# Kernel optimization log

Measured on AMD Instinct MI355X. Metric: run time of the kernel, lower is better.

The kernel has to match this reference:

```python
import jax, jax.numpy as jnp
import numpy as np

N_ENT = 100000
N_REL = 100
DIM = 128
N_BASES = 10
N_LAYERS = 2
N_EDGES = 600000


def setup_inputs() -> dict:
    key = jax.random.key(0)
    ks = jax.random.split(key, 8)
    source = jax.random.randint(ks[0], (N_EDGES,), 0, N_ENT)
    target = jax.random.randint(ks[1], (N_EDGES,), 0, N_ENT)
    edge_type = jax.random.randint(ks[2], (N_EDGES,), 0, N_REL)
    x0 = jax.random.normal(ks[3], (N_ENT, DIM), dtype=jnp.float32)
    bases = jax.random.normal(ks[4], (N_BASES, DIM, DIM), dtype=jnp.float32) * (DIM ** -0.5)
    coefs = jax.random.normal(ks[5], (N_LAYERS, N_REL, N_BASES), dtype=jnp.float32) * (N_BASES ** -0.5)
    self_w = jax.random.normal(ks[6], (N_LAYERS, DIM, DIM), dtype=jnp.float32) * (DIM ** -0.5)
    bias = jnp.zeros((N_LAYERS, DIM), dtype=jnp.float32)
    return {"x0": x0, "bases": bases, "coefs": coefs, "self_w": self_w,
            "bias": bias, "source": source, "target": target, "edge_type": edge_type}


def reference(x0, bases, coefs, self_w, bias, source, target, edge_type):
    """R-GCN entity representations (basis decomposition, inverse in-degree norm).

    x0: (N, d) base entity embeddings; bases: (B, d, d); coefs: (L, R, B);
    self_w: (L, d, d); bias: (L, d); source/target/edge_type: (E,) int.
    Returns (N, d) entity representations after L layers.
    """
    n = x0.shape[0]
    n_layers = coefs.shape[0]
    n_bases = bases.shape[0]
    # inverse in-degree edge weights: w_e = 1 / indegree(target_e)
    indeg = jax.ops.segment_sum(jnp.ones_like(target, dtype=x0.dtype), target, num_segments=n)
    ew = (1.0 / jnp.maximum(indeg, 1.0))[target]  # (E,)
    x = x0
    for l in range(n_layers):
        xs = x[source]                         # (E, d) gather
        ecoef = coefs[l][edge_type]            # (E, B) relation-specific basis coefficients
        msg = jnp.zeros_like(xs)
        for b in range(n_bases):               # small fixed loop over bases
            msg = msg + ecoef[:, b:b + 1] * (xs @ bases[b])
        agg = jax.ops.segment_sum(ew[:, None] * msg, target, num_segments=n)  # (N, d)
        x = jax.nn.relu(agg + x @ self_w[l] + bias[l])
    return x
```

## Files before the change

kernel.cpp:

```cpp
#include <hip/hip_runtime.h>

#define NENT    100000
#define NENTPAD 100096
#define NREL    100
#define DIM     128
#define NBASES  10
#define NEDGES  600000
#define CH      128
#define TMAX    4788
#define PADE    612736
#define NB_ESCAN 98
#define EPB     4096
#define NBH     147

typedef unsigned short u16;
typedef unsigned int   u32;
typedef __bf16  bf16x8 __attribute__((ext_vector_type(8)));
typedef float   f32x16 __attribute__((ext_vector_type(16)));

static __device__ __forceinline__ u16 f2bf(float f) {
  u32 u = __float_as_uint(f);
  u = (u + 0x7fffu + ((u >> 16) & 1u)) >> 16;
  return (u16)u;
}
static __device__ __forceinline__ float bf2f(u32 h) {
  return __uint_as_float(h << 16);
}
static __device__ __forceinline__ u32 pk2(float a, float b) {
  return (u32)f2bf(a) | ((u32)f2bf(b) << 16);
}
#define GLD16(g, l) __builtin_amdgcn_global_load_lds( \
    (__attribute__((address_space(1))) u32*)(g), \
    (__attribute__((address_space(3))) u32*)(l), 16, 0, 0)

__global__ __launch_bounds__(1024) void k_hist2(const int* __restrict__ tgt,
                                                const int* __restrict__ rel,
                                                int* __restrict__ indeg,
                                                int* __restrict__ hist) {
  __shared__ int h[NREL];
  int tid = threadIdx.x, blk = blockIdx.x;
  if (tid < NREL) h[tid] = 0;
  __syncthreads();
  int base = blk * EPB;
  int nv = NEDGES - base; if (nv > EPB) nv = EPB;
#pragma unroll
  for (int k = 0; k < 4; ++k) {
    int j = tid + k * 1024;
    if (j < nv) {
      int i = base + j;
      atomicAdd(&indeg[tgt[i]], 1);
      atomicAdd(&h[rel[i]], 1);
    }
  }
  __syncthreads();
  if (tid < NREL) hist[tid * NBH + blk] = h[tid];
}

__global__ __launch_bounds__(1024) void k_scan2(int* __restrict__ hist,
                                                int* __restrict__ chunk_rel,
                                                int* __restrict__ chunk_start,
                                                int* __restrict__ chunk_valid,
                                                int* __restrict__ chunkT) {
  __shared__ int sh[NREL * NBH];
  __shared__ int cnt[NREL];
  __shared__ int cb[128];
  int tid = threadIdx.x;
  for (int i = tid; i < NREL * NBH; i += 1024) sh[i] = hist[i];
  __syncthreads();
  if (tid < NREL) {
    int s = 0;
    for (int b = 0; b < NBH; ++b) s += sh[tid * NBH + b];
    cnt[tid] = s;
  }
  __syncthreads();
  if (tid < 128) cb[tid] = (tid < NREL) ? (cnt[tid] + CH - 1) / CH : 0;
  __syncthreads();
  for (int d = 1; d < 128; d <<= 1) {
    int t = 0;
    if (tid < 128 && tid >= d) t = cb[tid - d];
    __syncthreads();
    if (tid < 128) cb[tid] += t;
    __syncthreads();
  }
  if (tid < NREL) {
    int c = cnt[tid];
    int nch = (c + CH - 1) / CH;
    int cb0 = cb[tid] - nch;
    int poff = cb0 * CH;
    for (int i = 0; i < nch; ++i) {
      chunk_rel[cb0 + i] = tid;
      chunk_start[cb0 + i] = (cb0 + i) * CH;
      int v = c - i * CH;
      if (v > CH) v = CH;
      chunk_valid[cb0 + i] = v;
    }
    int run = poff;
    for (int b = 0; b < NBH; ++b) {
      int t = sh[tid * NBH + b];
      sh[tid * NBH + b] = run;
      run += t;
    }
  }
  if (tid == 127) *chunkT = cb[127];
  __syncthreads();
  for (int i = tid; i < NREL * NBH; i += 1024) hist[i] = sh[i];
}

__global__ __launch_bounds__(1024) void k_scatter2(const int* __restrict__ src,
                                                   const int* __restrict__ tgt,
                                                   const int* __restrict__ rel,
                                                   const int* __restrict__ hist,
                                                   const int* __restrict__ row_ptr,
                                                   int* __restrict__ fill_t,
                                                   int* __restrict__ es,
                                                   int* __restrict__ tp) {
  __shared__ int lh[NREL];
  __shared__ int lc[NREL];
  __shared__ int goff[NREL];
  __shared__ int ls[128];
  __shared__ int es_l[EPB];
  __shared__ int tp_l[EPB];
  __shared__ int dst_l[EPB];
  int tid = threadIdx.x, blk = blockIdx.x;
  int base = blk * EPB;
  int nv = NEDGES - base; if (nv > EPB) nv = EPB;
  if (tid < NREL) {
    lh[tid] = 0; lc[tid] = 0;
    goff[tid] = hist[tid * NBH + blk];
  }
  __syncthreads();
  int r4[4], s4[4], t4[4];
#pragma unroll
  for (int k = 0; k < 4; ++k) {
    int j = tid + k * 1024;
    if (j < nv) {
      int i = base + j;
      r4[k] = rel[i]; s4[k] = src[i]; t4[k] = tgt[i];
      atomicAdd(&lh[r4[k]], 1);
    } else r4[k] = -1;
  }
  __syncthreads();
  if (tid < 128) ls[tid] = (tid < NREL) ? lh[tid] : 0;
  __syncthreads();
  for (int d = 1; d < 128; d <<= 1) {
    int t = 0;
    if (tid < 128 && tid >= d) t = ls[tid - d];
    __syncthreads();
    if (tid < 128) ls[tid] += t;
    __syncthreads();
  }
#pragma unroll
  for (int k = 0; k < 4; ++k) {
    if (r4[k] >= 0) {
      int r = r4[k];
      int rank = atomicAdd(&lc[r], 1);
      int lpos = ls[r] - lh[r] + rank;
      es_l[lpos] = s4[k];
      dst_l[lpos] = goff[r] + rank;
      tp_l[lpos] = row_ptr[t4[k]] + atomicAdd(&fill_t[t4[k]], 1);
    }
  }
  __syncthreads();
  for (int j = tid; j < nv; j += 1024) {
    int d = dst_l[j];
    es[d] = es_l[j];
    tp[d] = tp_l[j];
  }
}

__global__ void k_escanA(const int* __restrict__ indeg, int* __restrict__ loc,
                         int* __restrict__ bsum) {
  __shared__ int s[256];
  int tid = threadIdx.x;
  int base = blockIdx.x * 1024 + tid * 4;
  int v0 = (base + 0 < NENT) ? indeg[base + 0] : 0;
  int v1 = (base + 1 < NENT) ? indeg[base + 1] : 0;
  int v2 = (base + 2 < NENT) ? indeg[base + 2] : 0;
  int v3 = (base + 3 < NENT) ? indeg[base + 3] : 0;
  s[tid] = v0 + v1 + v2 + v3;
  __syncthreads();
  for (int d = 1; d < 256; d <<= 1) {
    int t = (tid >= d) ? s[tid - d] : 0;
    __syncthreads();
    s[tid] += t;
    __syncthreads();
  }
  int off = (tid > 0) ? s[tid - 1] : 0;
  if (base + 0 < NENT) loc[base + 0] = off;
  if (base + 1 < NENT) loc[base + 1] = off + v0;
  if (base + 2 < NENT) loc[base + 2] = off + v0 + v1;
  if (base + 3 < NENT) loc[base + 3] = off + v0 + v1 + v2;
  if (tid == 255) bsum[blockIdx.x] = s[255];
}

__global__ void k_escanB(int* __restrict__ bsum) {
  __shared__ int s[128];
  int tid = threadIdx.x;
  s[tid] = (tid < NB_ESCAN) ? bsum[tid] : 0;
  __syncthreads();
  for (int d = 1; d < 128; d <<= 1) {
    int t = (tid >= d) ? s[tid - d] : 0;
    __syncthreads();
    s[tid] += t;
    __syncthreads();
  }
  if (tid < NB_ESCAN) bsum[tid] = (tid > 0) ? s[tid - 1] : 0;
}

__global__ void k_escanC(const int* __restrict__ loc, const int* __restrict__ bsum,
                         int* __restrict__ row_ptr) {
  int i = blockIdx.x * blockDim.x + threadIdx.x;
  if (i < NENT) row_ptr[i] = loc[i] + bsum[i >> 10];
}

__global__ void k_tobf(const float* __restrict__ x, u16* __restrict__ xbf) {
  int t = blockIdx.x * 256 + threadIdx.x;
  int row = t >> 4, g = t & 15;
  int c = g ^ (row & 7);
  const float4* xr = (const float4*)(x + (size_t)row * DIM + c * 8);
  float4 a = xr[0], b = xr[1];
  uint4 o;
  o.x = pk2(a.x, a.y); o.y = pk2(a.z, a.w);
  o.z = pk2(b.x, b.y); o.w = pk2(b.z, b.w);
  *(uint4*)(xbf + (size_t)row * DIM + g * 8) = o;
}

__global__ void k_wmatT(const float* __restrict__ bases, const float* __restrict__ coefs_l,
                        u16* __restrict__ Wt) {
  int g = blockIdx.x * 256 + threadIdx.x;
  int r = g >> 11;
  int rem = g & 2047;
  int k8 = rem >> 7;
  int dim = rem & 127;
  float cf[NBASES];
#pragma unroll
  for (int bb = 0; bb < NBASES; ++bb) cf[bb] = coefs_l[r * NBASES + bb];
  float v[8];
#pragma unroll
  for (int i = 0; i < 8; ++i) v[i] = 0.f;
  for (int bb = 0; bb < NBASES; ++bb) {
    const float* bp = bases + (size_t)bb * DIM * DIM + (k8 * 8) * DIM + dim;
#pragma unroll
    for (int i = 0; i < 8; ++i) v[i] += cf[bb] * bp[i * DIM];
  }
  uint4 o;
  o.x = pk2(v[0], v[1]); o.y = pk2(v[2], v[3]);
  o.z = pk2(v[4], v[5]); o.w = pk2(v[6], v[7]);
  *(uint4*)(Wt + (size_t)r * DIM * DIM + dim * DIM + ((k8 ^ (dim & 7)) * 8)) = o;
}

__global__ void k_swtT(const float* __restrict__ sw, u16* __restrict__ swt) {
  int g = blockIdx.x * 256 + threadIdx.x;
  int ll = g >> 11;
  int rem = g & 2047;
  int k8 = rem >> 7;
  int dim = rem & 127;
  const float* bp = sw + (size_t)ll * DIM * DIM + (k8 * 8) * DIM + dim;
  float v[8];
#pragma unroll
  for (int i = 0; i < 8; ++i) v[i] = bp[i * DIM];
  uint4 o;
  o.x = pk2(v[0], v[1]); o.y = pk2(v[2], v[3]);
  o.z = pk2(v[4], v[5]); o.w = pk2(v[6], v[7]);
  *(uint4*)(swt + (size_t)ll * DIM * DIM + dim * DIM + ((k8 ^ (dim & 7)) * 8)) = o;
}

__launch_bounds__(512, 4)
__global__ void k_edgeM(const u16* __restrict__ xbf, const u16* __restrict__ Wt,
                        const int* __restrict__ es, const int* __restrict__ tp,
                        const int* __restrict__ chunk_rel, const int* __restrict__ chunk_start,
                        const int* __restrict__ chunk_valid, const int* __restrict__ chunkT,
                        u16* __restrict__ msg) {
  __shared__ __align__(16) char smem[65536];
  int b = blockIdx.x;
  if (b >= *chunkT) return;
  int tid = threadIdx.x;
  int r = chunk_rel[b], base = chunk_start[b], nv = chunk_valid[b];
  {
    const char* wg = (const char*)(Wt + (size_t)r * DIM * DIM);
#pragma unroll
    for (int it = 0; it < 4; ++it) {
      int off = it * 8192 + tid * 16;
      GLD16(wg + off, smem + off);
    }
  }
  {
    int e = tid >> 2, q = tid & 3;
    int sidx = (e < nv) ? es[base + e] : 0;
    const char* xr = (const char*)(xbf + (size_t)sidx * DIM);
    char* xd = smem + 32768 + e * 256;
    int xk = (sidx & 7) ^ (e & 7);
#pragma unroll
    for (int i = 0; i < 4; ++i) {
      int g = q * 4 + i;
      uint4 v = *(const uint4*)(xr + g * 16);
      *(uint4*)(xd + ((g ^ xk) * 16)) = v;
    }
  }
  __syncthreads();
  int w = tid >> 6, l = tid & 63;
  int lr = l & 31, hi = l >> 5;
  int dt = w & 3;
  int d = dt * 32 + lr;
  int e1 = (w >> 2) * 32 + lr;
  const char* wb = smem;
  const char* xb = smem + 32768;
  f32x16 accA, accB;
#pragma unroll
  for (int i = 0; i < 16; ++i) { accA[i] = 0.f; accB[i] = 0.f; }
  int aswz = d & 7, bswz = lr & 7;
#pragma unroll
  for (int s = 0; s < 8; ++s) {
    int c = s * 2 + hi;
    bf16x8 av = *(const bf16x8*)(wb + d * 256 + ((c ^ aswz) * 16));
    bf16x8 b1 = *(const bf16x8*)(xb + e1 * 256 + ((c ^ bswz) * 16));
    bf16x8 b2 = *(const bf16x8*)(xb + (e1 + 64) * 256 + ((c ^ bswz) * 16));
    accA = __builtin_amdgcn_mfma_f32_32x32x16_bf16(av, b1, accA, 0, 0, 0);
    accB = __builtin_amdgcn_mfma_f32_32x32x16_bf16(av, b2, accB, 0, 0, 0);
  }
#pragma unroll
  for (int t = 0; t < 2; ++t) {
    int e = e1 + t * 64;
    if (e < nv) {
      int p = tp[base + e];
      u16* mrow = msg + (size_t)p * DIM + dt * 32 + hi * 4;
#pragma unroll
      for (int q = 0; q < 4; ++q) {
        float v0 = t ? accB[4 * q + 0] : accA[4 * q + 0];
        float v1 = t ? accB[4 * q + 1] : accA[4 * q + 1];
        float v2 = t ? accB[4 * q + 2] : accA[4 * q + 2];
        float v3 = t ? accB[4 * q + 3] : accA[4 * q + 3];
        uint2 o;
        o.x = pk2(v0, v1); o.y = pk2(v2, v3);
        *(uint2*)(mrow + 8 * q) = o;
      }
    }
  }
}

__launch_bounds__(512, 4)
__global__ void k_combM(const u16* __restrict__ xbf, const u16* __restrict__ swt,
                        const float* __restrict__ bias_l, const u16* __restrict__ msg,
                        const int* __restrict__ row_ptr, const int* __restrict__ indeg,
                        float* __restrict__ outf, u16* __restrict__ outb, int last) {
  __shared__ __align__(16) char smem[65536];
  int tid = threadIdx.x;
  int r0 = blockIdx.x * 128;
  {
    const char* wg = (const char*)swt;
    const char* xg = (const char*)(xbf + (size_t)r0 * DIM);
#pragma unroll
    for (int it = 0; it < 4; ++it) {
      int off = it * 8192 + tid * 16;
      GLD16(wg + off, smem + off);
      GLD16(xg + off, smem + 32768 + off);
    }
  }
  __syncthreads();
  int w = tid >> 6, l = tid & 63;
  int lr = l & 31, hi = l >> 5;
  int dt = w & 3;
  int d = dt * 32 + lr;
  int e1 = (w >> 2) * 32 + lr;
  const char* wb = smem;
  const char* xb = smem + 32768;
  f32x16 accA, accB;
#pragma unroll
  for (int i = 0; i < 16; ++i) { accA[i] = 0.f; accB[i] = 0.f; }
  int aswz = d & 7, bswz = lr & 7;
#pragma unroll
  for (int s = 0; s < 8; ++s) {
    int c = s * 2 + hi;
    bf16x8 av = *(const bf16x8*)(wb + d * 256 + ((c ^ aswz) * 16));
    bf16x8 b1 = *(const bf16x8*)(xb + e1 * 256 + ((c ^ bswz) * 16));
    bf16x8 b2 = *(const bf16x8*)(xb + (e1 + 64) * 256 + ((c ^ bswz) * 16));
    accA = __builtin_amdgcn_mfma_f32_32x32x16_bf16(av, b1, accA, 0, 0, 0);
    accB = __builtin_amdgcn_mfma_f32_32x32x16_bf16(av, b2, accB, 0, 0, 0);
  }
#pragma unroll
  for (int t = 0; t < 2; ++t) {
    int ent = r0 + e1 + t * 64;
    int vald = (ent < NENT);
    int eb = vald ? row_ptr[ent] : 0;
    int dg = vald ? indeg[ent] : 0;
    float inv = 1.f / (float)(dg > 1 ? dg : 1);
    float ms[16];
#pragma unroll
    for (int i = 0; i < 16; ++i) ms[i] = 0.f;
    const u16* mp = msg + (size_t)eb * DIM + dt * 32 + hi * 4;
    for (int j = 0; j < dg; ++j) {
#pragma unroll
      for (int q = 0; q < 4; ++q) {
        uint2 m = *(const uint2*)(mp + 8 * q);
        ms[4 * q + 0] += bf2f(m.x & 0xffffu);
        ms[4 * q + 1] += bf2f(m.x >> 16);
        ms[4 * q + 2] += bf2f(m.y & 0xffffu);
        ms[4 * q + 3] += bf2f(m.y >> 16);
      }
      mp += DIM;
    }
    if (vald) {
#pragma unroll
      for (int q = 0; q < 4; ++q) {
        float4 bi = *(const float4*)(bias_l + dt * 32 + hi * 4 + 8 * q);
        float a0 = t ? accB[4 * q + 0] : accA[4 * q + 0];
        float a1 = t ? accB[4 * q + 1] : accA[4 * q + 1];
        float a2 = t ? accB[4 * q + 2] : accA[4 * q + 2];
        float a3 = t ? accB[4 * q + 3] : accA[4 * q + 3];
        float o0 = fmaxf(ms[4 * q + 0] * inv + a0 + bi.x, 0.f);
        float o1 = fmaxf(ms[4 * q + 1] * inv + a1 + bi.y, 0.f);
        float o2 = fmaxf(ms[4 * q + 2] * inv + a2 + bi.z, 0.f);
        float o3 = fmaxf(ms[4 * q + 3] * inv + a3 + bi.w, 0.f);
        if (last) {
          float4 o = make_float4(o0, o1, o2, o3);
          *(float4*)(outf + (size_t)ent * DIM + dt * 32 + hi * 4 + 8 * q) = o;
        } else {
          int c16 = 4 * dt + q;
          uint2 o;
          o.x = pk2(o0, o1); o.y = pk2(o2, o3);
          *(uint2*)(outb + (size_t)ent * DIM + ((c16 ^ (ent & 7)) * 8) + 4 * hi) = o;
        }
      }
    }
  }
}

extern "C" void kernel_launch(void* const* d_in, const int* in_sizes, int n_in,
                              void* d_out, int out_size, void* d_ws, size_t ws_size,
                              hipStream_t stream) {
  const float* x0    = (const float*)d_in[0];
  const float* bases = (const float*)d_in[1];
  const float* coefs = (const float*)d_in[2];
  const float* selfw = (const float*)d_in[3];
  const float* bias  = (const float*)d_in[4];
  const int* src = (const int*)d_in[5];
  const int* tgt = (const int*)d_in[6];
  const int* rel = (const int*)d_in[7];
  float* out = (float*)d_out;

  char* ws = (char*)d_ws;
  size_t off = 0;
  auto alloc = [&](size_t bytes) -> void* {
    void* p = ws + off;
    off = (off + bytes + 255) & ~(size_t)255;
    return p;
  };
  u16* Wt   = (u16*)alloc((size_t)NREL * DIM * DIM * 2);
  u16* swt  = (u16*)alloc((size_t)2 * DIM * DIM * 2);
  u16* xbf  = (u16*)alloc((size_t)NENTPAD * DIM * 2);
  u16* msg  = (u16*)alloc((size_t)NEDGES * DIM * 2);
  int* es      = (int*)alloc((size_t)PADE * sizeof(int));
  int* tp      = (int*)alloc((size_t)PADE * sizeof(int));
  int* indeg   = (int*)alloc((size_t)NENT * sizeof(int));
  int* row_ptr = (int*)alloc((size_t)NENT * sizeof(int));
  int* loc     = (int*)alloc((size_t)NENT * sizeof(int));
  int* fill_t  = (int*)alloc((size_t)NENT * sizeof(int));
  int* bsum    = (int*)alloc(128 * sizeof(int));
  int* hist    = (int*)alloc((size_t)NREL * NBH * sizeof(int));
  int* chunk_rel   = (int*)alloc(TMAX * sizeof(int));
  int* chunk_start = (int*)alloc(TMAX * sizeof(int));
  int* chunk_valid = (int*)alloc(TMAX * sizeof(int));
  int* chunkT      = (int*)alloc(sizeof(int));

  hipMemsetAsync(indeg, 0, (size_t)NENT * sizeof(int), stream);
  hipMemsetAsync(fill_t, 0, (size_t)NENT * sizeof(int), stream);

  k_hist2<<<NBH, 1024, 0, stream>>>(tgt, rel, indeg, hist);
  k_scan2<<<1, 1024, 0, stream>>>(hist, chunk_rel, chunk_start, chunk_valid, chunkT);
  k_escanA<<<NB_ESCAN, 256, 0, stream>>>(indeg, loc, bsum);
  k_escanB<<<1, 128, 0, stream>>>(bsum);
  k_escanC<<<(NENT + 255) / 256, 256, 0, stream>>>(loc, bsum, row_ptr);
  k_scatter2<<<NBH, 1024, 0, stream>>>(src, tgt, rel, hist, row_ptr, fill_t, es, tp);
  k_tobf<<<(NENT * 16) / 256, 256, 0, stream>>>(x0, xbf);
  k_swtT<<<16, 256, 0, stream>>>(selfw, swt);

  for (int l = 0; l < 2; ++l) {
    k_wmatT<<<(NREL * 2048) / 256, 256, 0, stream>>>(bases, coefs + l * NREL * NBASES, Wt);
    k_edgeM<<<TMAX, 512, 0, stream>>>(xbf, Wt, es, tp,
                                      chunk_rel, chunk_start, chunk_valid, chunkT, msg);
    k_combM<<<NENTPAD / 128, 512, 0, stream>>>(xbf, swt + (size_t)l * DIM * DIM,
                                               bias + l * DIM, msg, row_ptr, indeg,
                                               out, xbf, l == 0 ? 0 : 1);
  }
}
```

Before: 398.3 us.

## Load weight fragments into registers, halve LDS, swizzle X during direct global-to-LDS load

In the edge and combine kernels, each wave now loads its weight-matrix MFMA A-fragments straight from global memory into registers, so they are no longer staged in LDS. The X tile is copied with direct global-to-LDS loads whose source addresses apply the XOR swizzle, and the stored bf16 layouts become plain row-major. LDS per block drops from 64KB to 32KB and launch bounds rise to 6 blocks, aiming for higher occupancy and less LDS traffic. In exchange each wave issues its own weight loads (more global/L2 traffic) and needs more VGPRs.

Result: slower. 438.5 us (+10.1%).

```diff
diff --git a/kernel.cpp b/kernel.cpp
--- a/kernel.cpp
+++ b/kernel.cpp
@@ -215,14 +215,12 @@
 
 __global__ void k_tobf(const float* __restrict__ x, u16* __restrict__ xbf) {
   int t = blockIdx.x * 256 + threadIdx.x;
-  int row = t >> 4, g = t & 15;
-  int c = g ^ (row & 7);
-  const float4* xr = (const float4*)(x + (size_t)row * DIM + c * 8);
+  const float4* xr = (const float4*)(x + (size_t)t * 8);
   float4 a = xr[0], b = xr[1];
   uint4 o;
   o.x = pk2(a.x, a.y); o.y = pk2(a.z, a.w);
   o.z = pk2(b.x, b.y); o.w = pk2(b.z, b.w);
-  *(uint4*)(xbf + (size_t)row * DIM + g * 8) = o;
+  *(uint4*)(xbf + (size_t)t * 8) = o;
 }
 
 __global__ void k_wmatT(const float* __restrict__ bases, const float* __restrict__ coefs_l,
@@ -246,7 +244,7 @@
   uint4 o;
   o.x = pk2(v[0], v[1]); o.y = pk2(v[2], v[3]);
   o.z = pk2(v[4], v[5]); o.w = pk2(v[6], v[7]);
-  *(uint4*)(Wt + (size_t)r * DIM * DIM + dim * DIM + ((k8 ^ (dim & 7)) * 8)) = o;
+  *(uint4*)(Wt + (size_t)r * DIM * DIM + dim * DIM + k8 * 8) = o;
 }
 
 __global__ void k_swtT(const float* __restrict__ sw, u16* __restrict__ swt) {
@@ -262,61 +260,53 @@
   uint4 o;
   o.x = pk2(v[0], v[1]); o.y = pk2(v[2], v[3]);
   o.z = pk2(v[4], v[5]); o.w = pk2(v[6], v[7]);
-  *(uint4*)(swt + (size_t)ll * DIM * DIM + dim * DIM + ((k8 ^ (dim & 7)) * 8)) = o;
-}
-
-__launch_bounds__(512, 4)
+  *(uint4*)(swt + (size_t)ll * DIM * DIM + dim * DIM + k8 * 8) = o;
+}
+
+__launch_bounds__(512, 6)
 __global__ void k_edgeM(const u16* __restrict__ xbf, const u16* __restrict__ Wt,
                         const int* __restrict__ es, const int* __restrict__ tp,
                         const int* __restrict__ chunk_rel, const int* __restrict__ chunk_start,
                         const int* __restrict__ chunk_valid, const int* __restrict__ chunkT,
                         u16* __restrict__ msg) {
-  __shared__ __align__(16) char smem[65536];
+  __shared__ __align__(16) char smem[32768];
   int b = blockIdx.x;
   if (b >= *chunkT) return;
   int tid = threadIdx.x;
   int r = chunk_rel[b], base = chunk_start[b], nv = chunk_valid[b];
-  {
-    const char* wg = (const char*)(Wt + (size_t)r * DIM * DIM);
-#pragma unroll
-    for (int it = 0; it < 4; ++it) {
-      int off = it * 8192 + tid * 16;
-      GLD16(wg + off, smem + off);
-    }
-  }
-  {
-    int e = tid >> 2, q = tid & 3;
-    int sidx = (e < nv) ? es[base + e] : 0;
-    const char* xr = (const char*)(xbf + (size_t)sidx * DIM);
-    char* xd = smem + 32768 + e * 256;
-    int xk = (sidx & 7) ^ (e & 7);
-#pragma unroll
-    for (int i = 0; i < 4; ++i) {
-      int g = q * 4 + i;
-      uint4 v = *(const uint4*)(xr + g * 16);
-      *(uint4*)(xd + ((g ^ xk) * 16)) = v;
-    }
-  }
-  __syncthreads();
   int w = tid >> 6, l = tid & 63;
   int lr = l & 31, hi = l >> 5;
   int dt = w & 3;
   int d = dt * 32 + lr;
+  const char* wgb = (const char*)(Wt + (size_t)r * DIM * DIM) + d * 256 + hi * 16;
+  bf16x8 av[8];
+#pragma unroll
+  for (int s = 0; s < 8; ++s) av[s] = *(const bf16x8*)(wgb + s * 32);
+  {
+    char* ldst = smem + (tid >> 6) * 4096 + (tid & 63) * 16;
+#pragma unroll
+    for (int j = 0; j < 4; ++j) {
+      int row = w * 16 + j * 4 + (l >> 4);
+      int srow = (row < nv) ? es[base + row] : 0;
+      const char* gsrc = (const char*)(xbf + (size_t)srow * DIM)
+                         + (((l & 15) ^ (row & 7)) * 16);
+      GLD16(gsrc, ldst + j * 1024);
+    }
+  }
+  __syncthreads();
   int e1 = (w >> 2) * 32 + lr;
-  const char* wb = smem;
-  const char* xb = smem + 32768;
+  const char* xb = smem;
   f32x16 accA, accB;
 #pragma unroll
   for (int i = 0; i < 16; ++i) { accA[i] = 0.f; accB[i] = 0.f; }
-  int aswz = d & 7, bswz = lr & 7;
+  int bswz = e1 & 7;
 #pragma unroll
   for (int s = 0; s < 8; ++s) {
     int c = s * 2 + hi;
-    bf16x8 av = *(const bf16x8*)(wb + d * 256 + ((c ^ aswz) * 16));
     bf16x8 b1 = *(const bf16x8*)(xb + e1 * 256 + ((c ^ bswz) * 16));
     bf16x8 b2 = *(const bf16x8*)(xb + (e1 + 64) * 256 + ((c ^ bswz) * 16));
-    accA = __builtin_amdgcn_mfma_f32_32x32x16_bf16(av, b1, accA, 0, 0, 0);
-    accB = __builtin_amdgcn_mfma_f32_32x32x16_bf16(av, b2, accB, 0, 0, 0);
+    accA = __builtin_amdgcn_mfma_f32_32x32x16_bf16(av[s], b1, accA, 0, 0, 0);
+    accB = __builtin_amdgcn_mfma_f32_32x32x16_bf16(av[s], b2, accB, 0, 0, 0);
   }
 #pragma unroll
   for (int t = 0; t < 2; ++t) {
@@ -338,44 +328,46 @@
   }
 }
 
-__launch_bounds__(512, 4)
+__launch_bounds__(512, 6)
 __global__ void k_combM(const u16* __restrict__ xbf, const u16* __restrict__ swt,
                         const float* __restrict__ bias_l, const u16* __restrict__ msg,
                         const int* __restrict__ row_ptr, const int* __restrict__ indeg,
                         float* __restrict__ outf, u16* __restrict__ outb, int last) {
-  __shared__ __align__(16) char smem[65536];
+  __shared__ __align__(16) char smem[32768];
   int tid = threadIdx.x;
   int r0 = blockIdx.x * 128;
-  {
-    const char* wg = (const char*)swt;
-    const char* xg = (const char*)(xbf + (size_t)r0 * DIM);
-#pragma unroll
-    for (int it = 0; it < 4; ++it) {
-      int off = it * 8192 + tid * 16;
-      GLD16(wg + off, smem + off);
-      GLD16(xg + off, smem + 32768 + off);
-    }
-  }
-  __syncthreads();
   int w = tid >> 6, l = tid & 63;
   int lr = l & 31, hi = l >> 5;
   int dt = w & 3;
   int d = dt * 32 + lr;
+  const char* wgb = (const char*)swt + d * 256 + hi * 16;
+  bf16x8 av[8];
+#pragma unroll
+  for (int s = 0; s < 8; ++s) av[s] = *(const bf16x8*)(wgb + s * 32);
+  {
+    char* ldst = smem + (tid >> 6) * 4096 + (tid & 63) * 16;
+#pragma unroll
+    for (int j = 0; j < 4; ++j) {
+      int row = w * 16 + j * 4 + (l >> 4);
+      const char* gsrc = (const char*)(xbf + (size_t)(r0 + row) * DIM)
+                         + (((l & 15) ^ (row & 7)) * 16);
+      GLD16(gsrc, ldst + j * 1024);
+    }
+  }
+  __syncthreads();
   int e1 = (w >> 2) * 32 + lr;
-  const char* wb = smem;
-  const char* xb = smem + 32768;
+  const char* xb = smem;
   f32x16 accA, accB;
 #pragma unroll
   for (int i = 0; i < 16; ++i) { accA[i] = 0.f; accB[i] = 0.f; }
-  int aswz = d & 7, bswz = lr & 7;
+  int bswz = e1 & 7;
 #pragma unroll
   for (int s = 0; s < 8; ++s) {
     int c = s * 2 + hi;
-    bf16x8 av = *(const bf16x8*)(wb + d * 256 + ((c ^ aswz) * 16));
     bf16x8 b1 = *(const bf16x8*)(xb + e1 * 256 + ((c ^ bswz) * 16));
     bf16x8 b2 = *(const bf16x8*)(xb + (e1 + 64) * 256 + ((c ^ bswz) * 16));
-    accA = __builtin_amdgcn_mfma_f32_32x32x16_bf16(av, b1, accA, 0, 0, 0);
-    accB = __builtin_amdgcn_mfma_f32_32x32x16_bf16(av, b2, accB, 0, 0, 0);
+    accA = __builtin_amdgcn_mfma_f32_32x32x16_bf16(av[s], b1, accA, 0, 0, 0);
+    accB = __builtin_amdgcn_mfma_f32_32x32x16_bf16(av[s], b2, accB, 0, 0, 0);
   }
 #pragma unroll
   for (int t = 0; t < 2; ++t) {
@@ -415,10 +407,9 @@
           float4 o = make_float4(o0, o1, o2, o3);
           *(float4*)(outf + (size_t)ent * DIM + dt * 32 + hi * 4 + 8 * q) = o;
         } else {
-          int c16 = 4 * dt + q;
           uint2 o;
           o.x = pk2(o0, o1); o.y = pk2(o2, o3);
-          *(uint2*)(outb + (size_t)ent * DIM + ((c16 ^ (ent & 7)) * 8) + 4 * hi) = o;
+          *(uint2*)(outb + (size_t)ent * DIM + dt * 32 + 8 * q + 4 * hi) = o;
         }
       }
     }
@@ -471,7 +462,7 @@
   k_escanB<<<1, 128, 0, stream>>>(bsum);
   k_escanC<<<(NENT + 255) / 256, 256, 0, stream>>>(loc, bsum, row_ptr);
   k_scatter2<<<NBH, 1024, 0, stream>>>(src, tgt, rel, hist, row_ptr, fill_t, es, tp);
-  k_tobf<<<(NENT * 16) / 256, 256, 0, stream>>>(x0, xbf);
+  k_tobf<<<(NENT * DIM / 8) / 256, 256, 0, stream>>>(x0, xbf);
   k_swtT<<<16, 256, 0, stream>>>(selfw, swt);
 
   for (int l = 0; l < 2; ++l) {
```

## Drop LDS staging in edge kernel; load fragments directly into registers

Applied to the files above, without the earlier changes.

The edge message kernel no longer stages the relation weight and gathered source rows in shared memory. Each wave now loads its 32 edges' source-row fragments straight into registers and computes all four 32-wide output tiles, reading weight fragments from global memory in a pre-permuted layout that the weight-build kernel now writes. The edge chunk size doubles to 256, so each block handles more edges per relation and there are fewer blocks. This removes the LDS round trip and the barrier, but adds repeated global/L2 reads of the weight matrix per wave, higher register pressure, and more padding from larger chunks.

New measurement: 607.0 us. +52.4%, slower.

```diff
diff --git a/kernel.cpp b/kernel.cpp
--- a/kernel.cpp
+++ b/kernel.cpp
@@ -6,9 +6,9 @@
 #define DIM     128
 #define NBASES  10
 #define NEDGES  600000
-#define CH      128
-#define TMAX    4788
-#define PADE    612736
+#define CH      256
+#define TMAX    2448
+#define PADE    625664
 #define NB_ESCAN 98
 #define EPB     4096
 #define NBH     147
@@ -230,8 +230,10 @@
   int g = blockIdx.x * 256 + threadIdx.x;
   int r = g >> 11;
   int rem = g & 2047;
-  int k8 = rem >> 7;
-  int dim = rem & 127;
+  int d = rem >> 4;
+  int hi = (rem >> 3) & 1;
+  int s = rem & 7;
+  int k8 = 2 * s + hi;
   float cf[NBASES];
 #pragma unroll
   for (int bb = 0; bb < NBASES; ++bb) cf[bb] = coefs_l[r * NBASES + bb];
@@ -239,14 +241,14 @@
 #pragma unroll
   for (int i = 0; i < 8; ++i) v[i] = 0.f;
   for (int bb = 0; bb < NBASES; ++bb) {
-    const float* bp = bases + (size_t)bb * DIM * DIM + (k8 * 8) * DIM + dim;
+    const float* bp = bases + (size_t)bb * DIM * DIM + (k8 * 8) * DIM + d;
 #pragma unroll
     for (int i = 0; i < 8; ++i) v[i] += cf[bb] * bp[i * DIM];
   }
   uint4 o;
   o.x = pk2(v[0], v[1]); o.y = pk2(v[2], v[3]);
   o.z = pk2(v[4], v[5]); o.w = pk2(v[6], v[7]);
-  *(uint4*)(Wt + (size_t)r * DIM * DIM + dim * DIM + ((k8 ^ (dim & 7)) * 8)) = o;
+  *(uint4*)(Wt + (size_t)r * 16384 + d * 128 + hi * 64 + s * 8) = o;
 }
 
 __global__ void k_swtT(const float* __restrict__ sw, u16* __restrict__ swt) {
@@ -271,68 +273,45 @@
                         const int* __restrict__ chunk_rel, const int* __restrict__ chunk_start,
                         const int* __restrict__ chunk_valid, const int* __restrict__ chunkT,
                         u16* __restrict__ msg) {
-  __shared__ __align__(16) char smem[65536];
   int b = blockIdx.x;
   if (b >= *chunkT) return;
   int tid = threadIdx.x;
   int r = chunk_rel[b], base = chunk_start[b], nv = chunk_valid[b];
-  {
-    const char* wg = (const char*)(Wt + (size_t)r * DIM * DIM);
-#pragma unroll
-    for (int it = 0; it < 4; ++it) {
-      int off = it * 8192 + tid * 16;
-      GLD16(wg + off, smem + off);
-    }
-  }
-  {
-    int e = tid >> 2, q = tid & 3;
-    int sidx = (e < nv) ? es[base + e] : 0;
-    const char* xr = (const char*)(xbf + (size_t)sidx * DIM);
-    char* xd = smem + 32768 + e * 256;
-    int xk = (sidx & 7) ^ (e & 7);
-#pragma unroll
-    for (int i = 0; i < 4; ++i) {
-      int g = q * 4 + i;
-      uint4 v = *(const uint4*)(xr + g * 16);
-      *(uint4*)(xd + ((g ^ xk) * 16)) = v;
-    }
-  }
-  __syncthreads();
   int w = tid >> 6, l = tid & 63;
   int lr = l & 31, hi = l >> 5;
-  int dt = w & 3;
-  int d = dt * 32 + lr;
-  int e1 = (w >> 2) * 32 + lr;
-  const char* wb = smem;
-  const char* xb = smem + 32768;
-  f32x16 accA, accB;
-#pragma unroll
-  for (int i = 0; i < 16; ++i) { accA[i] = 0.f; accB[i] = 0.f; }
-  int aswz = d & 7, bswz = lr & 7;
-#pragma unroll
-  for (int s = 0; s < 8; ++s) {
-    int c = s * 2 + hi;
-    bf16x8 av = *(const bf16x8*)(wb + d * 256 + ((c ^ aswz) * 16));
-    bf16x8 b1 = *(const bf16x8*)(xb + e1 * 256 + ((c ^ bswz) * 16));
-    bf16x8 b2 = *(const bf16x8*)(xb + (e1 + 64) * 256 + ((c ^ bswz) * 16));
-    accA = __builtin_amdgcn_mfma_f32_32x32x16_bf16(av, b1, accA, 0, 0, 0);
-    accB = __builtin_amdgcn_mfma_f32_32x32x16_bf16(av, b2, accB, 0, 0, 0);
-  }
-#pragma unroll
-  for (int t = 0; t < 2; ++t) {
-    int e = e1 + t * 64;
-    if (e < nv) {
-      int p = tp[base + e];
-      u16* mrow = msg + (size_t)p * DIM + dt * 32 + hi * 4;
+  int e = w * 32 + lr;
+  int srow = (e < nv) ? es[base + e] : 0;
+  const char* xr = (const char*)(xbf + (size_t)srow * DIM);
+  int key = srow & 7;
+  bf16x8 bfr[8];
+#pragma unroll
+  for (int s = 0; s < 8; ++s)
+    bfr[s] = *(const bf16x8*)(xr + (((2 * s + hi) ^ key) * 16));
+  const char* wB = (const char*)Wt + (size_t)r * 32768;
+  f32x16 acc[4];
+#pragma unroll
+  for (int dt = 0; dt < 4; ++dt) {
+    const char* ab = wB + (dt * 32 + lr) * 256 + hi * 128;
+    bf16x8 av[8];
+#pragma unroll
+    for (int s = 0; s < 8; ++s) av[s] = *(const bf16x8*)(ab + s * 16);
+#pragma unroll
+    for (int i = 0; i < 16; ++i) acc[dt][i] = 0.f;
+#pragma unroll
+    for (int s = 0; s < 8; ++s)
+      acc[dt] = __builtin_amdgcn_mfma_f32_32x32x16_bf16(av[s], bfr[s], acc[dt], 0, 0, 0);
+  }
+  if (e < nv) {
+    int p = tp[base + e];
+    u16* mrow = msg + (size_t)p * DIM + hi * 4;
+#pragma unroll
+    for (int dt = 0; dt < 4; ++dt) {
 #pragma unroll
       for (int q = 0; q < 4; ++q) {
-        float v0 = t ? accB[4 * q + 0] : accA[4 * q + 0];
-        float v1 = t ? accB[4 * q + 1] : accA[4 * q + 1];
-        float v2 = t ? accB[4 * q + 2] : accA[4 * q + 2];
-        float v3 = t ? accB[4 * q + 3] : accA[4 * q + 3];
         uint2 o;
-        o.x = pk2(v0, v1); o.y = pk2(v2, v3);
-        *(uint2*)(mrow + 8 * q) = o;
+        o.x = pk2(acc[dt][4 * q + 0], acc[dt][4 * q + 1]);
+        o.y = pk2(acc[dt][4 * q + 2], acc[dt][4 * q + 3]);
+        *(uint2*)(mrow + dt * 32 + q * 8) = o;
       }
     }
   }
```
